# Optimization experiments

Hardware: AMD Instinct MI355X
Metric: run time of the kernel (lower is better)

The kernel has to match this reference:

```python
import jax, jax.numpy as jnp
import numpy as np

N_NODES, N_EDGES, DIM = 50000, 800000, 128


def setup_inputs() -> dict:
    key = jax.random.key(0)
    ks = jax.random.split(key, 16)
    s = 1.0 / np.sqrt(DIM)
    inp = {
        "x": jax.random.normal(ks[0], (N_NODES, DIM), dtype=jnp.float32),
        "edge_index": jax.random.randint(ks[1], (2, N_EDGES), 0, N_NODES, dtype=jnp.int64),
    }
    # 3 GIN layers, each with a 2-layer MLP (Linear-ReLU-Linear)
    for i in range(3):
        inp[f"w1_{i}"] = jax.random.normal(ks[2 + 4 * i], (DIM, DIM), dtype=jnp.float32) * s
        inp[f"b1_{i}"] = jnp.zeros((DIM,), dtype=jnp.float32)
        inp[f"w2_{i}"] = jax.random.normal(ks[3 + 4 * i], (DIM, DIM), dtype=jnp.float32) * s
        inp[f"b2_{i}"] = jnp.zeros((DIM,), dtype=jnp.float32)
    inp["wh"] = jax.random.normal(ks[14], (DIM, DIM), dtype=jnp.float32) * s
    inp["bh"] = jnp.zeros((DIM,), dtype=jnp.float32)
    return inp


def _gin_layer(h, src, dst, w1, b1, w2, b2, residual):
    # message passing: gather x[src], scatter-add at dst (aggr='sum')
    neigh = jax.ops.segment_sum(h[src], dst, num_segments=h.shape[0])
    out = h + neigh  # (1 + eps) * x + neigh, eps = 0
    out = jnp.maximum(out @ w1 + b1, 0.0) @ w2 + b2  # MLP (dropout p=0)
    if residual:  # res_fc is Identity since in_dim == out_dim
        out = out + h
    return out


def reference(x, edge_index, w1_0, b1_0, w2_0, b2_0, w1_1, b1_1, w2_1, b2_1,
              w1_2, b1_2, w2_2, b2_2, wh, bh):
    src, dst = edge_index[0], edge_index[1]
    h = x
    h = _gin_layer(h, src, dst, w1_0, b1_0, w2_0, b2_0, residual=True)
    h = _gin_layer(h, src, dst, w1_1, b1_1, w2_1, b2_1, residual=True)
    # last layer: encoding=False -> no residual
    h = _gin_layer(h, src, dst, w1_2, b1_2, w2_2, b2_2, residual=False)
    # extra_output_fc head
    return h @ wh + bh
```

## Files before the change

kernel.cpp:

```cpp
#include <hip/hip_runtime.h>
#include <hip/hip_fp16.h>

#define N_NODES 50000
#define N_EDGES 800000
#define DIM 128
#define FEAT_ELEMS (N_NODES * DIM)
#define STRIDE 64
#define NB 391
#define BCAP 3072

typedef __attribute__((ext_vector_type(8))) _Float16 f16x8;
typedef __attribute__((ext_vector_type(4))) float f32x4;
typedef __attribute__((ext_vector_type(2))) float f32x2;

#define MFMA_F16 __builtin_amdgcn_mfma_f32_16x16x32_f16


__global__ __launch_bounds__(256) void prep_combo_kernel(
    const float* __restrict__ w0, const float* __restrict__ w1,
    const float* __restrict__ w2, const float* __restrict__ w3,
    const float* __restrict__ w4, const float* __restrict__ w5,
    const float* __restrict__ w6, __half* __restrict__ dst,
    const float* __restrict__ x, __half* __restrict__ hm,
    unsigned char* __restrict__ qm, int* __restrict__ gcnt) {
    const int b = blockIdx.x;
    if (b < 112) {
        const int wsel = b >> 4;
        const int chunk = b & 15;
        const float* W;
        switch (wsel) {
            case 0: W = w0; break;
            case 1: W = w1; break;
            case 2: W = w2; break;
            case 3: W = w3; break;
            case 4: W = w4; break;
            case 5: W = w5; break;
            default: W = w6; break;
        }
        __half* d = dst + (size_t)wsel * 16384;
        int idx = chunk * 1024 + threadIdx.x;
#pragma unroll
        for (int t = 0; t < 4; ++t, idx += 256) {
            int k = idx >> 7, n = idx & 127;
            int ks = k >> 5, q = (k >> 3) & 3, j = k & 7;
            int ct = n >> 4, c = n & 15;
            int lane = q * 16 + c;
            int base = ((ks * 8 + ct) * 64 + lane) * 8 + j;
            d[base] = __float2half(W[idx]);
        }
    } else if (b < 1136) {
        int i = (b - 112) * 256 + threadIdx.x;
        const int stride = 1024 * 256;
        const int n4 = FEAT_ELEMS / 4;
        for (; i < n4; i += stride) {
            float4 v = ((const float4*)x)[i];
            __half2 h0 = __floats2half2_rn(v.x, v.y);
            __half2 h1 = __floats2half2_rn(v.z, v.w);
            uint2 u;
            u.x = *(unsigned*)&h0;
            u.y = *(unsigned*)&h1;
            ((uint2*)hm)[i] = u;
            int p = __builtin_amdgcn_cvt_pk_fp8_f32(v.x, v.y, 0, false);
            p = __builtin_amdgcn_cvt_pk_fp8_f32(v.z, v.w, p, true);
            ((int*)qm)[i] = p;
        }
    } else {
        for (int i = threadIdx.x; i < NB; i += 256) gcnt[i] = 0;
    }
}


__global__ __launch_bounds__(256) void bucket_kernel(const int* __restrict__ ei,
                                                     int* __restrict__ gcnt,
                                                     long long* __restrict__ ebuf) {
    __shared__ int hist[NB];
    __shared__ int base[NB];
    __shared__ int sh_is64;
    const int tid = threadIdx.x;
    for (int i = tid; i < NB; i += 256) hist[i] = 0;
    if (tid == 0) {
        int o = 0;
        for (int i = 1; i < 64; i += 2) o |= ei[i];
        sh_is64 = (o == 0) ? 1 : 0;
    }
    __syncthreads();
    const int e0 = blockIdx.x * 2048;
    const int is64 = sh_is64;
    int sv[8], dv[8];
    int nl = 0;
#pragma unroll
    for (int k = 0; k < 8; ++k) {
        int e = e0 + k * 256 + tid;
        if (e < N_EDGES) {
            int s = is64 ? ei[2 * e] : ei[e];
            int d = is64 ? ei[2 * (N_EDGES + e)] : ei[N_EDGES + e];
            sv[nl] = s;
            dv[nl] = d;
            atomicAdd(&hist[d >> 7], 1);
            ++nl;
        }
    }
    __syncthreads();
    for (int i = tid; i < NB; i += 256) {
        int h = hist[i];
        base[i] = h ? atomicAdd(&gcnt[i], h) : 0;
    }
    __syncthreads();
    for (int i = tid; i < NB; i += 256) hist[i] = 0;
    __syncthreads();
    for (int k = 0; k < nl; ++k) {
        int b = dv[k] >> 7;
        int r = base[b] + atomicAdd(&hist[b], 1);
        if (r < BCAP)
            ebuf[(size_t)b * BCAP + r] = ((long long)sv[k] << 32) | (unsigned)dv[k];
    }
}


__global__ __launch_bounds__(256) void build_kernel(const int* __restrict__ gcnt,
                                                    const long long* __restrict__ ebuf,
                                                    int* __restrict__ cnt,
                                                    int* __restrict__ col_idx) {
    __shared__ int cur[128];
    const int b = blockIdx.x;
    const int tid = threadIdx.x;
    if (tid < 128) cur[tid] = 0;
    __syncthreads();
    int n = gcnt[b];
    if (n > BCAP) n = BCAP;
    const long long* eb = ebuf + (size_t)b * BCAP;
    for (int i = tid; i < n; i += 256) {
        long long p = eb[i];
        int d = (int)(p & 0xFFFFFFFFll);
        int s = (int)(p >> 32);
        int slot = atomicAdd(&cur[d & 127], 1);
        if (slot < STRIDE) col_idx[d * STRIDE + slot] = s;
    }
    __syncthreads();
    int node = b * 128 + tid;
    if (tid < 128 && node < N_NODES) {
        int c = cur[tid];
        cnt[node] = (c > STRIDE) ? STRIDE : c;
    }
}


template <bool LAST>
__global__ __launch_bounds__(256, 4) void gin_layer_kernel(
    const __half* __restrict__ Hs,
    const unsigned char* __restrict__ Qm,
    const int* __restrict__ cnt,
    const int* __restrict__ col_idx,
    const __half* __restrict__ W1f,
    const __half* __restrict__ W2f,
    const __half* __restrict__ Whf,
    const float* __restrict__ b1,
    const float* __restrict__ b2,
    const float* __restrict__ bh,
    __half* __restrict__ Hout,
    unsigned char* __restrict__ Qout,
    float* __restrict__ Cout) {
    __shared__ __align__(16) __half ul[4][2048];
    const int tid = threadIdx.x;
    const int lane = tid & 63;
    const int wid = tid >> 6;
    const int c = lane & 15;
    const int q = lane >> 4;
    const int R = (blockIdx.x * 4 + wid) * 16;
    if (R >= N_NODES) return;

    {
        const int d0 = c * 8;
#define ACCQ(U)                                                             \
    {                                                                       \
        f32x2 g0 = __builtin_amdgcn_cvt_pk_f32_fp8((int)(U).x, false);      \
        f32x2 g1 = __builtin_amdgcn_cvt_pk_f32_fp8((int)(U).x, true);       \
        f32x2 g2 = __builtin_amdgcn_cvt_pk_f32_fp8((int)(U).y, false);      \
        f32x2 g3 = __builtin_amdgcn_cvt_pk_f32_fp8((int)(U).y, true);       \
        acc[0] += g0.x; acc[1] += g0.y; acc[2] += g1.x; acc[3] += g1.y;     \
        acc[4] += g2.x; acc[5] += g2.y; acc[6] += g3.x; acc[7] += g3.y;     \
    }
#pragma unroll
        for (int it = 0; it < 4; ++it) {
            const int rl = it * 4 + q;
            const size_t grow = (size_t)(R + rl);
            float acc[8];
            {
                uint4 sv = *(const uint4*)(Hs + grow * DIM + d0);
                const __half2* sp = (const __half2*)&sv;
                float2 s0 = __half22float2(sp[0]), s1 = __half22float2(sp[1]);
                float2 s2 = __half22float2(sp[2]), s3 = __half22float2(sp[3]);
                acc[0] = s0.x; acc[1] = s0.y; acc[2] = s1.x; acc[3] = s1.y;
                acc[4] = s2.x; acc[5] = s2.y; acc[6] = s3.x; acc[7] = s3.y;
            }
            int d = cnt[grow];
            if (d > STRIDE) d = STRIDE;
            const int* ci = col_idx + grow * STRIDE;
            int j = 0;
            for (; j + 8 <= d; j += 8) {
                int s[8];
#pragma unroll
                for (int k = 0; k < 8; ++k) s[k] = ci[j + k];
                uint2 u[8];
#pragma unroll
                for (int k = 0; k < 8; ++k)
                    u[k] = *(const uint2*)(Qm + (size_t)s[k] * DIM + d0);
#pragma unroll
                for (int k = 0; k < 8; ++k) ACCQ(u[k])
            }
            for (; j + 2 <= d; j += 2) {
                int s0 = ci[j], s1 = ci[j + 1];
                uint2 u0 = *(const uint2*)(Qm + (size_t)s0 * DIM + d0);
                uint2 u1 = *(const uint2*)(Qm + (size_t)s1 * DIM + d0);
                ACCQ(u0)
                ACCQ(u1)
            }
            if (j < d) {
                int s = ci[j];
                uint2 u = *(const uint2*)(Qm + (size_t)s * DIM + d0);
                ACCQ(u)
            }
            uint4 o;
            __half2* op = (__half2*)&o;
            op[0] = __floats2half2_rn(acc[0], acc[1]);
            op[1] = __floats2half2_rn(acc[2], acc[3]);
            op[2] = __floats2half2_rn(acc[4], acc[5]);
            op[3] = __floats2half2_rn(acc[6], acc[7]);
            *(uint4*)&ul[wid][rl * 128 + (d0 ^ ((rl & 7) << 3))] = o;
        }
#undef ACCQ
    }

    f16x8 a[4];
#pragma unroll
    for (int ks = 0; ks < 4; ++ks)
        a[ks] = *(const f16x8*)&ul[wid][c * 128 + ((ks * 32 + q * 8) ^ ((c & 7) << 3))];

    f32x4 acc1[8];
#pragma unroll
    for (int ct = 0; ct < 8; ++ct) acc1[ct] = (f32x4){0.f, 0.f, 0.f, 0.f};
#pragma unroll
    for (int ks = 0; ks < 4; ++ks) {
#pragma unroll
        for (int ct = 0; ct < 8; ++ct) {
            f16x8 b = *(const f16x8*)(W1f + (ks * 8 + ct) * 512 + lane * 8);
            acc1[ct] = MFMA_F16(a[ks], b, acc1[ct], 0, 0, 0);
        }
    }

#pragma unroll
    for (int ct = 0; ct < 8; ++ct) {
        const int col = ct * 16 + c;
        const float bv = b1[col];
#pragma unroll
        for (int rr = 0; rr < 4; ++rr) {
            const int rl = q * 4 + rr;
            ul[wid][rl * 128 + (col ^ ((rl & 7) << 3))] =
                __float2half(fmaxf(acc1[ct][rr] + bv, 0.f));
        }
    }

    f32x4 acc2[8];
#pragma unroll
    for (int ct = 0; ct < 8; ++ct) acc2[ct] = (f32x4){0.f, 0.f, 0.f, 0.f};
#pragma unroll
    for (int ks = 0; ks < 4; ++ks) {
        f16x8 ua = *(const f16x8*)&ul[wid][c * 128 + ((ks * 32 + q * 8) ^ ((c & 7) << 3))];
#pragma unroll
        for (int ct = 0; ct < 8; ++ct) {
            f16x8 b = *(const f16x8*)(W2f + (ks * 8 + ct) * 512 + lane * 8);
            acc2[ct] = MFMA_F16(ua, b, acc2[ct], 0, 0, 0);
        }
    }

#pragma unroll
    for (int ct = 0; ct < 8; ++ct) {
        const int col = ct * 16 + c;
        const float bv = b2[col];
#pragma unroll
        for (int rr = 0; rr < 4; ++rr) {
            const int rl = q * 4 + rr;
            ul[wid][rl * 128 + (col ^ (q << 4))] = __float2half(acc2[ct][rr] + bv);
        }
    }

    if (!LAST) {
        const int row2 = lane >> 2;
        const int cb = (lane & 3) * 8;
        const size_t grow = (size_t)(R + row2);
#pragma unroll
        for (int k = 0; k < 4; ++k) {
            const int c0 = cb + k * 32;
            uint4 hv = *(uint4*)&ul[wid][row2 * 128 + (c0 ^ ((row2 >> 2) << 4))];
            const __half2* hp = (const __half2*)&hv;
            float2 t0 = __half22float2(hp[0]), t1 = __half22float2(hp[1]);
            float2 t2 = __half22float2(hp[2]), t3 = __half22float2(hp[3]);
            float f0 = t0.x, f1 = t0.y, f2 = t1.x, f3 = t1.y;
            float f4 = t2.x, f5 = t2.y, f6 = t3.x, f7 = t3.y;
            {
                uint4 rv = *(const uint4*)(Hs + grow * DIM + c0);
                const __half2* rp = (const __half2*)&rv;
                float2 r0 = __half22float2(rp[0]), r1 = __half22float2(rp[1]);
                float2 r2 = __half22float2(rp[2]), r3 = __half22float2(rp[3]);
                f0 += r0.x; f1 += r0.y; f2 += r1.x; f3 += r1.y;
                f4 += r2.x; f5 += r2.y; f6 += r3.x; f7 += r3.y;
            }
            uint4 ov;
            __half2* op = (__half2*)&ov;
            op[0] = __floats2half2_rn(f0, f1);
            op[1] = __floats2half2_rn(f2, f3);
            op[2] = __floats2half2_rn(f4, f5);
            op[3] = __floats2half2_rn(f6, f7);
            *(uint4*)(Hout + grow * DIM + c0) = ov;
            int q0 = __builtin_amdgcn_cvt_pk_fp8_f32(f0, f1, 0, false);
            q0 = __builtin_amdgcn_cvt_pk_fp8_f32(f2, f3, q0, true);
            int q1 = __builtin_amdgcn_cvt_pk_fp8_f32(f4, f5, 0, false);
            q1 = __builtin_amdgcn_cvt_pk_fp8_f32(f6, f7, q1, true);
            uint2 qv;
            qv.x = (unsigned)q0;
            qv.y = (unsigned)q1;
            *(uint2*)(Qout + grow * DIM + c0) = qv;
        }
    } else {
        f32x4 acc3[8];
#pragma unroll
        for (int ct = 0; ct < 8; ++ct) acc3[ct] = (f32x4){0.f, 0.f, 0.f, 0.f};
#pragma unroll
        for (int ks = 0; ks < 4; ++ks) {
            f16x8 ha =
                *(const f16x8*)&ul[wid][c * 128 + ((ks * 32 + q * 8) ^ ((c >> 2) << 4))];
#pragma unroll
            for (int ct = 0; ct < 8; ++ct) {
                f16x8 b = *(const f16x8*)(Whf + (ks * 8 + ct) * 512 + lane * 8);
                acc3[ct] = MFMA_F16(ha, b, acc3[ct], 0, 0, 0);
            }
        }
#pragma unroll
        for (int ct = 0; ct < 8; ++ct) {
            const int col = ct * 16 + c;
            const float bv = bh[col];
#pragma unroll
            for (int rr = 0; rr < 4; ++rr) {
                const int row = R + q * 4 + rr;
                Cout[(size_t)row * DIM + col] = acc3[ct][rr] + bv;
            }
        }
    }
}


extern "C" void kernel_launch(void* const* d_in, const int* in_sizes, int n_in,
                              void* d_out, int out_size, void* d_ws, size_t ws_size,
                              hipStream_t stream) {
    const float* x = (const float*)d_in[0];
    const int* ei = (const int*)d_in[1];
    const float* w1[3] = {(const float*)d_in[2], (const float*)d_in[6], (const float*)d_in[10]};
    const float* b1[3] = {(const float*)d_in[3], (const float*)d_in[7], (const float*)d_in[11]};
    const float* w2[3] = {(const float*)d_in[4], (const float*)d_in[8], (const float*)d_in[12]};
    const float* b2[3] = {(const float*)d_in[5], (const float*)d_in[9], (const float*)d_in[13]};
    const float* wh = (const float*)d_in[14];
    const float* bh = (const float*)d_in[15];
    float* out = (float*)d_out;

    char* ws = (char*)d_ws;
    const size_t HFEAT = (size_t)FEAT_ELEMS * sizeof(__half);
    const size_t QFEAT = (size_t)FEAT_ELEMS;
    size_t off = 0;
    int* cnt = (int*)(ws + off);                         off += 200704;
    int* col_idx = (int*)(ws + off);                     off += (size_t)N_NODES * STRIDE * 4;
    int* gcnt = (int*)(ws + off);                        off += 4096;
    __half* Wf = (__half*)(ws + off);                    off += 7 * 32768;
    long long* ebuf = (long long*)(ws + off);            off += (size_t)NB * BCAP * 8;
    __half* HMx = (__half*)(ws + off);                   off += HFEAT;
    __half* HM1 = (__half*)(ws + off);                   off += HFEAT;
    __half* HM0 = (__half*)(ws + off);                   off += HFEAT;
    unsigned char* Qx = (unsigned char*)(ws + off);      off += QFEAT;
    unsigned char* Q1 = (unsigned char*)(ws + off);      off += QFEAT;
    unsigned char* Q0 = (unsigned char*)(ws + off);      off += QFEAT;

    const int GIN_BLKS = (N_NODES / 16 + 3) / 4;

    prep_combo_kernel<<<1137, 256, 0, stream>>>(w1[0], w2[0], w1[1], w2[1], w1[2], w2[2],
                                                wh, Wf, x, HMx, Qx, gcnt);
    bucket_kernel<<<NB, 256, 0, stream>>>(ei, gcnt, ebuf);
    build_kernel<<<NB, 256, 0, stream>>>(gcnt, ebuf, cnt, col_idx);

#define WF(i) (Wf + (size_t)(i) * 16384)

    gin_layer_kernel<false><<<GIN_BLKS, 256, 0, stream>>>(
        HMx, Qx, cnt, col_idx, WF(0), WF(1), nullptr, b1[0], b2[0], nullptr,
        HM1, Q1, nullptr);

    gin_layer_kernel<false><<<GIN_BLKS, 256, 0, stream>>>(
        HM1, Q1, cnt, col_idx, WF(2), WF(3), nullptr, b1[1], b2[1], nullptr,
        HM0, Q0, nullptr);

    gin_layer_kernel<true><<<GIN_BLKS, 256, 0, stream>>>(
        HM0, Q0, cnt, col_idx, WF(4), WF(5), WF(6), b1[2], b2[2], bh,
        nullptr, nullptr, out);
#undef WF
}
```

Baseline: 237.1 us.

## Split each 16-row GIN tile across two waves sharing LDS tiles

Each block now handles one 16-row tile with 128 threads (two waves). The two waves split the aggregation rows and the output column tiles of every MFMA GEMM, exchanging intermediates through shared LDS buffers with block barriers. This halves the per-wave accumulator count and the weight loads per wave, and doubles the number of waves working on gathers, which should raise parallelism and lower register pressure. In exchange it adds three __syncthreads per layer and duplicates the A-fragment LDS reads across both waves.

```diff
diff --git a/kernel.cpp b/kernel.cpp
--- a/kernel.cpp
+++ b/kernel.cpp
@@ -146,7 +146,7 @@
 
 
 template <bool LAST>
-__global__ __launch_bounds__(256, 4) void gin_layer_kernel(
+__global__ __launch_bounds__(128, 4) void gin_layer_kernel(
     const __half* __restrict__ Hs,
     const unsigned char* __restrict__ Qm,
     const int* __restrict__ cnt,
@@ -160,17 +160,18 @@
     __half* __restrict__ Hout,
     unsigned char* __restrict__ Qout,
     float* __restrict__ Cout) {
-    __shared__ __align__(16) __half ul[4][2048];
+    __shared__ __align__(16) __half tl[2048];
+    __shared__ __align__(16) __half ul[2048];
     const int tid = threadIdx.x;
     const int lane = tid & 63;
     const int wid = tid >> 6;
     const int c = lane & 15;
     const int q = lane >> 4;
-    const int R = (blockIdx.x * 4 + wid) * 16;
-    if (R >= N_NODES) return;
+    const int R = blockIdx.x * 16;
 
     {
-        const int d0 = c * 8;
+        const int g = tid >> 4;
+        const int d0 = (tid & 15) * 8;
 #define ACCQ(U)                                                             \
     {                                                                       \
         f32x2 g0 = __builtin_amdgcn_cvt_pk_f32_fp8((int)(U).x, false);      \
@@ -181,8 +182,8 @@
         acc[4] += g2.x; acc[5] += g2.y; acc[6] += g3.x; acc[7] += g3.y;     \
     }
 #pragma unroll
-        for (int it = 0; it < 4; ++it) {
-            const int rl = it * 4 + q;
+        for (int it = 0; it < 2; ++it) {
+            const int rl = it * 8 + g;
             const size_t grow = (size_t)(R + rl);
             float acc[8];
             {
@@ -226,72 +227,77 @@
             op[1] = __floats2half2_rn(acc[2], acc[3]);
             op[2] = __floats2half2_rn(acc[4], acc[5]);
             op[3] = __floats2half2_rn(acc[6], acc[7]);
-            *(uint4*)&ul[wid][rl * 128 + (d0 ^ ((rl & 7) << 3))] = o;
+            *(uint4*)&tl[rl * 128 + (d0 ^ ((rl & 7) << 3))] = o;
         }
 #undef ACCQ
     }
+    __syncthreads();
 
     f16x8 a[4];
 #pragma unroll
     for (int ks = 0; ks < 4; ++ks)
-        a[ks] = *(const f16x8*)&ul[wid][c * 128 + ((ks * 32 + q * 8) ^ ((c & 7) << 3))];
-
-    f32x4 acc1[8];
-#pragma unroll
-    for (int ct = 0; ct < 8; ++ct) acc1[ct] = (f32x4){0.f, 0.f, 0.f, 0.f};
+        a[ks] = *(const f16x8*)&tl[c * 128 + ((ks * 32 + q * 8) ^ ((c & 7) << 3))];
+
+    f32x4 acc1[4];
+#pragma unroll
+    for (int t = 0; t < 4; ++t) acc1[t] = (f32x4){0.f, 0.f, 0.f, 0.f};
 #pragma unroll
     for (int ks = 0; ks < 4; ++ks) {
 #pragma unroll
-        for (int ct = 0; ct < 8; ++ct) {
-            f16x8 b = *(const f16x8*)(W1f + (ks * 8 + ct) * 512 + lane * 8);
-            acc1[ct] = MFMA_F16(a[ks], b, acc1[ct], 0, 0, 0);
-        }
-    }
-
-#pragma unroll
-    for (int ct = 0; ct < 8; ++ct) {
-        const int col = ct * 16 + c;
+        for (int t = 0; t < 4; ++t) {
+            const int ctg = wid * 4 + t;
+            f16x8 b = *(const f16x8*)(W1f + (ks * 8 + ctg) * 512 + lane * 8);
+            acc1[t] = MFMA_F16(a[ks], b, acc1[t], 0, 0, 0);
+        }
+    }
+
+#pragma unroll
+    for (int t = 0; t < 4; ++t) {
+        const int col = (wid * 4 + t) * 16 + c;
         const float bv = b1[col];
 #pragma unroll
         for (int rr = 0; rr < 4; ++rr) {
             const int rl = q * 4 + rr;
-            ul[wid][rl * 128 + (col ^ ((rl & 7) << 3))] =
-                __float2half(fmaxf(acc1[ct][rr] + bv, 0.f));
-        }
-    }
-
-    f32x4 acc2[8];
-#pragma unroll
-    for (int ct = 0; ct < 8; ++ct) acc2[ct] = (f32x4){0.f, 0.f, 0.f, 0.f};
+            ul[rl * 128 + (col ^ ((rl & 7) << 3))] =
+                __float2half(fmaxf(acc1[t][rr] + bv, 0.f));
+        }
+    }
+    __syncthreads();
+
+    f32x4 acc2[4];
+#pragma unroll
+    for (int t = 0; t < 4; ++t) acc2[t] = (f32x4){0.f, 0.f, 0.f, 0.f};
 #pragma unroll
     for (int ks = 0; ks < 4; ++ks) {
-        f16x8 ua = *(const f16x8*)&ul[wid][c * 128 + ((ks * 32 + q * 8) ^ ((c & 7) << 3))];
-#pragma unroll
-        for (int ct = 0; ct < 8; ++ct) {
-            f16x8 b = *(const f16x8*)(W2f + (ks * 8 + ct) * 512 + lane * 8);
-            acc2[ct] = MFMA_F16(ua, b, acc2[ct], 0, 0, 0);
-        }
-    }
-
-#pragma unroll
-    for (int ct = 0; ct < 8; ++ct) {
-        const int col = ct * 16 + c;
+        f16x8 ua = *(const f16x8*)&ul[c * 128 + ((ks * 32 + q * 8) ^ ((c & 7) << 3))];
+#pragma unroll
+        for (int t = 0; t < 4; ++t) {
+            const int ctg = wid * 4 + t;
+            f16x8 b = *(const f16x8*)(W2f + (ks * 8 + ctg) * 512 + lane * 8);
+            acc2[t] = MFMA_F16(ua, b, acc2[t], 0, 0, 0);
+        }
+    }
+
+#pragma unroll
+    for (int t = 0; t < 4; ++t) {
+        const int col = (wid * 4 + t) * 16 + c;
         const float bv = b2[col];
 #pragma unroll
         for (int rr = 0; rr < 4; ++rr) {
             const int rl = q * 4 + rr;
-            ul[wid][rl * 128 + (col ^ (q << 4))] = __float2half(acc2[ct][rr] + bv);
-        }
-    }
+            tl[rl * 128 + (col ^ (q << 4))] = __float2half(acc2[t][rr] + bv);
+        }
+    }
+    __syncthreads();
 
     if (!LAST) {
-        const int row2 = lane >> 2;
-        const int cb = (lane & 3) * 8;
+        const int row2 = tid >> 3;
+        const int cb = (tid & 7) * 8;
         const size_t grow = (size_t)(R + row2);
 #pragma unroll
-        for (int k = 0; k < 4; ++k) {
-            const int c0 = cb + k * 32;
-            uint4 hv = *(uint4*)&ul[wid][row2 * 128 + (c0 ^ ((row2 >> 2) << 4))];
+        for (int k = 0; k < 2; ++k) {
+            const int c0 = cb + k * 64;
+            uint4 hv = *(uint4*)&tl[row2 * 128 + (c0 ^ ((row2 >> 2) << 4))];
             const __half2* hp = (const __half2*)&hv;
             float2 t0 = __half22float2(hp[0]), t1 = __half22float2(hp[1]);
             float2 t2 = __half22float2(hp[2]), t3 = __half22float2(hp[3]);
@@ -322,27 +328,28 @@
             *(uint2*)(Qout + grow * DIM + c0) = qv;
         }
     } else {
-        f32x4 acc3[8];
-#pragma unroll
-        for (int ct = 0; ct < 8; ++ct) acc3[ct] = (f32x4){0.f, 0.f, 0.f, 0.f};
+        f32x4 acc3[4];
+#pragma unroll
+        for (int t = 0; t < 4; ++t) acc3[t] = (f32x4){0.f, 0.f, 0.f, 0.f};
 #pragma unroll
         for (int ks = 0; ks < 4; ++ks) {
             f16x8 ha =
-                *(const f16x8*)&ul[wid][c * 128 + ((ks * 32 + q * 8) ^ ((c >> 2) << 4))];
-#pragma unroll
-            for (int ct = 0; ct < 8; ++ct) {
-                f16x8 b = *(const f16x8*)(Whf + (ks * 8 + ct) * 512 + lane * 8);
-                acc3[ct] = MFMA_F16(ha, b, acc3[ct], 0, 0, 0);
-            }
-        }
-#pragma unroll
-        for (int ct = 0; ct < 8; ++ct) {
-            const int col = ct * 16 + c;
+                *(const f16x8*)&tl[c * 128 + ((ks * 32 + q * 8) ^ ((c >> 2) << 4))];
+#pragma unroll
+            for (int t = 0; t < 4; ++t) {
+                const int ctg = wid * 4 + t;
+                f16x8 b = *(const f16x8*)(Whf + (ks * 8 + ctg) * 512 + lane * 8);
+                acc3[t] = MFMA_F16(ha, b, acc3[t], 0, 0, 0);
+            }
+        }
+#pragma unroll
+        for (int t = 0; t < 4; ++t) {
+            const int col = (wid * 4 + t) * 16 + c;
             const float bv = bh[col];
 #pragma unroll
             for (int rr = 0; rr < 4; ++rr) {
                 const int row = R + q * 4 + rr;
-                Cout[(size_t)row * DIM + col] = acc3[ct][rr] + bv;
+                Cout[(size_t)row * DIM + col] = acc3[t][rr] + bv;
             }
         }
     }
@@ -378,7 +385,7 @@
     unsigned char* Q1 = (unsigned char*)(ws + off);      off += QFEAT;
     unsigned char* Q0 = (unsigned char*)(ws + off);      off += QFEAT;
 
-    const int GIN_BLKS = (N_NODES / 16 + 3) / 4;
+    const int GIN_BLKS = N_NODES / 16;
 
     prep_combo_kernel<<<1137, 256, 0, stream>>>(w1[0], w2[0], w1[1], w2[1], w1[2], w2[2],
                                                 wh, Wf, x, HMx, Qx, gcnt);
@@ -387,15 +394,15 @@
 
 #define WF(i) (Wf + (size_t)(i) * 16384)
 
-    gin_layer_kernel<false><<<GIN_BLKS, 256, 0, stream>>>(
+    gin_layer_kernel<false><<<GIN_BLKS, 128, 0, stream>>>(
         HMx, Qx, cnt, col_idx, WF(0), WF(1), nullptr, b1[0], b2[0], nullptr,
         HM1, Q1, nullptr);
 
-    gin_layer_kernel<false><<<GIN_BLKS, 256, 0, stream>>>(
+    gin_layer_kernel<false><<<GIN_BLKS, 128, 0, stream>>>(
         HM1, Q1, cnt, col_idx, WF(2), WF(3), nullptr, b1[1], b2[1], nullptr,
         HM0, Q0, nullptr);
 
-    gin_layer_kernel<true><<<GIN_BLKS, 256, 0, stream>>>(
+    gin_layer_kernel<true><<<GIN_BLKS, 128, 0, stream>>>(
         HM0, Q0, cnt, col_idx, WF(4), WF(5), WF(6), b1[2], b2[2], bh,
         nullptr, nullptr, out);
 #undef WF
```

Result: faster. 230.7 us (-2.7%).
